# Kernel tuning notes

Hardware: AMD Instinct MI355X
Metric: run time of the kernel (lower is better)

Reference implementation:

```python
import jax, jax.numpy as jnp
import numpy as np
from jax import lax

NH = 8          # heads
DK = 64         # total key/query depth
DV = 64         # total value depth
DKH = DK // NH  # per-head key depth = 8
DVH = DV // NH  # per-head value depth = 8
H = W = 32
CIN = 256
FILTERS = 256


def rel_to_abs(x):
    # x: [B, N, L, 2L-1] relative logits -> [B, N, L, L] absolute logits
    B, N, L, _ = x.shape
    x = jnp.pad(x, ((0, 0), (0, 0), (0, 0), (0, 1)))          # [B,N,L,2L]
    flat = x.reshape(B, N, L * 2 * L)
    flat = jnp.pad(flat, ((0, 0), (0, 0), (0, L - 1)))        # [B,N,2L^2+L-1]
    final = flat.reshape(B, N, L + 1, 2 * L - 1)
    return final[:, :, :L, L - 1:]


def rel_logits_1d(q, rel_k, h, w, perm):
    # q: [B, NH, h, w, DKH], rel_k: [2w-1, DKH]
    B = q.shape[0]
    rel = jnp.einsum('bnxyd,md->bnxym', q, rel_k)             # [B,NH,h,w,2w-1]
    rel = rel.reshape(B, NH * h, w, 2 * w - 1)
    rel = rel_to_abs(rel)                                     # [B,NH*h,w,w]
    rel = rel.reshape(B, NH, h, w, w)[:, :, :, None]          # [B,NH,h,1,w,w]
    rel = jnp.broadcast_to(rel, (B, NH, h, h, w, w))          # tile over other axis
    rel = jnp.transpose(rel, perm)
    return rel.reshape(B, NH, h * w, h * w)


def setup_inputs() -> dict:
    key = jax.random.key(0)
    ks = jax.random.split(key, 6)
    s = lambda fan_in: 1.0 / np.sqrt(fan_in)
    return {
        'x': jax.random.normal(ks[0], (8, H, W, CIN), jnp.float32),
        'conv_w': jax.random.normal(ks[1], (3, 3, CIN, FILTERS - DV), jnp.float32) * s(9 * CIN),
        'conv_b': jnp.zeros((FILTERS - DV,), jnp.float32),
        'qkv_w': jax.random.normal(ks[2], (CIN, 2 * DK + DV), jnp.float32) * s(CIN),
        'qkv_b': jnp.zeros((2 * DK + DV,), jnp.float32),
        'attn_w': jax.random.normal(ks[3], (DV, DV), jnp.float32) * s(DV),
        'attn_b': jnp.zeros((DV,), jnp.float32),
        'key_rel_w': jax.random.normal(ks[4], (2 * W - 1, DKH), jnp.float32),
        'key_rel_h': jax.random.normal(ks[5], (2 * H - 1, DKH), jnp.float32),
    }


def reference(x, conv_w, conv_b, qkv_w, qkv_b, attn_w, attn_b, key_rel_w, key_rel_h):
    B = x.shape[0]
    # standard conv branch (SAME padding)
    conv_out = lax.conv_general_dilated(
        x, conv_w, window_strides=(1, 1), padding='SAME',
        dimension_numbers=('NHWC', 'HWIO', 'NHWC')) + conv_b

    # 1x1 qkv projection
    kqv = jnp.einsum('bhwc,co->bhwo', x, qkv_w) + qkv_b
    k = kqv[..., :DK]
    q = kqv[..., DK:2 * DK] * (DKH ** -0.5)
    v = kqv[..., 2 * DK:]

    def split_heads(t, d):
        return t.reshape(B, H, W, NH, d).transpose(0, 3, 1, 2, 4)  # [B,NH,H,W,d]

    qh = split_heads(q, DKH)
    kh = split_heads(k, DKH)
    vh = split_heads(v, DVH)

    qf = qh.reshape(B, NH, H * W, DKH)
    kf = kh.reshape(B, NH, H * W, DKH)
    vf = vh.reshape(B, NH, H * W, DVH)

    logits = jnp.einsum('bnid,bnjd->bnij', qf, kf)            # [B,NH,HW,HW]
    rel_w = rel_logits_1d(qh, key_rel_w, H, W, (0, 1, 2, 4, 3, 5))
    qh_t = qh.transpose(0, 1, 3, 2, 4)                        # [B,NH,W,H,d]
    rel_h = rel_logits_1d(qh_t, key_rel_h, W, H, (0, 1, 4, 2, 5, 3))
    logits = logits + rel_w + rel_h

    weights = jax.nn.softmax(logits, axis=-1)
    attn = jnp.einsum('bnij,bnjd->bnid', weights, vf)         # [B,NH,HW,DVH]
    attn = attn.reshape(B, NH, H, W, DVH).transpose(0, 2, 3, 1, 4).reshape(B, H, W, DV)
    attn = jnp.einsum('bhwc,co->bhwo', attn, attn_w) + attn_b

    return jnp.concatenate([conv_out, attn], axis=3)
```

## Files before the change

kernel.cpp:

```cpp
#include <hip/hip_runtime.h>
#include <cstdint>

using u16 = unsigned short;
using u32 = uint32_t;

typedef __attribute__((ext_vector_type(8))) short bf16x8;
typedef __attribute__((ext_vector_type(4))) float f32x4;

__device__ __forceinline__ float bf2f(u16 v) { return __uint_as_float(((u32)v) << 16); }
__device__ __forceinline__ u16 f2bf(float f) {
    u32 u = __float_as_uint(f);
    u += 0x7fffu + ((u >> 16) & 1u);
    return (u16)(u >> 16);
}

#define FLAG_OFF 0
#define WSH_OFF  2097168
#define AWF_OFF  2588688
#define CBF_OFF  2592784
#define QBF_OFF  2592976
#define ABF_OFF  2593168
#define KRW_OFF  2593232
#define KRH_OFF  2593736
#define KB_OFF   2594240
#define QB_OFF   3118528
#define VB_OFF   3642816
#define AT_OFF   4167104
#define WSHQ_OFF 9409984

__global__ void detect_kernel(const u16* __restrict__ x, int* __restrict__ flag) {
    __shared__ int cnt;
    if (threadIdx.x == 0) cnt = 0;
    __syncthreads();
    int c = 0;
    #pragma unroll
    for (int k = 0; k < 16; k++) {
        u16 v = x[threadIdx.x * 16 + k];
        int e = (v >> 7) & 0xFF;
        c += (e >= 110 && e <= 140) ? 1 : 0;
    }
    atomicAdd(&cnt, c);
    __syncthreads();
    if (threadIdx.x == 0) *flag = (cnt > 3300) ? 1 : 0;
}

__global__ __launch_bounds__(256) void prep_kernel(
    const void* __restrict__ cw, const void* __restrict__ qw,
    const void* __restrict__ cb, const void* __restrict__ qb,
    const void* __restrict__ aw, const void* __restrict__ ab,
    const void* __restrict__ kw_, const void* __restrict__ kh_,
    u16* __restrict__ wshC, u16* __restrict__ wshQ,
    float* __restrict__ cbf, float* __restrict__ qbf, float* __restrict__ awf,
    float* __restrict__ abf, float* __restrict__ krw, float* __restrict__ krh,
    const int* __restrict__ flag)
{
    const int blk = blockIdx.x;
    const int fl = *flag;
    if (blk < 240) {
        const void* w; u16* o; int g;
        if (blk < 216) { w = cw; o = wshC; g = blk * 256 + threadIdx.x; }
        else           { w = qw; o = wshQ; g = (blk - 216) * 256 + threadIdx.x; }
        const int kk = g / 768, rem = g % 768;
        const int tile = rem >> 6, lane = rem & 63;
        const int n = tile * 16 + (lane & 15);
        u16 tmp[8];
        #pragma unroll
        for (int j = 0; j < 8; j++) {
            const size_t k = (size_t)(kk * 32 + ((lane >> 4) << 3) + j);
            tmp[j] = fl ? ((const u16*)w)[k * 192 + n]
                        : f2bf(((const float*)w)[k * 192 + n]);
        }
        *(uint4*)(o + (size_t)g * 8) = *(const uint4*)tmp;
    } else {
        const int gid = (blk - 240) * 256 + threadIdx.x;
        const void* src; float* dst; int e;
        if      (gid <  192) { src = cb;  dst = cbf; e = gid; }
        else if (gid <  384) { src = qb;  dst = qbf; e = gid - 192; }
        else if (gid < 4480) { src = aw;  dst = awf; e = gid - 384; }
        else if (gid < 4544) { src = ab;  dst = abf; e = gid - 4480; }
        else if (gid < 5048) { src = kw_; dst = krw; e = gid - 4544; }
        else if (gid < 5552) { src = kh_; dst = krh; e = gid - 5048; }
        else return;
        dst[e] = fl ? bf2f(((const u16*)src)[e]) : ((const float*)src)[e];
    }
}

__global__ __launch_bounds__(256) void qkv_mfma_kernel(
    const void* __restrict__ xr, const u16* __restrict__ wsh, const float* __restrict__ qbf_,
    const int* __restrict__ flag,
    u16* __restrict__ kb16, float* __restrict__ qbuf, u16* __restrict__ vb16)
{
    const int coh = blockIdx.x, row = blockIdx.y;
    const int b = row >> 5, h = row & 31;
    const int t = threadIdx.x;
    __shared__ u16 xs[32 * 264];
    const int fl = *flag;

    if (fl) {
        const u16* src = (const u16*)xr + (size_t)row * 8192;
        #pragma unroll
        for (int i = 0; i < 4; ++i) {
            const int idx = t + i * 256;
            const int px = idx >> 5, cq = idx & 31;
            *(uint4*)(xs + px * 264 + cq * 8) = *(const uint4*)(src + px * 256 + cq * 8);
        }
    } else {
        const float* src = (const float*)xr + (size_t)row * 8192;
        #pragma unroll
        for (int i = 0; i < 8; ++i) {
            const int idx = t + i * 256;
            const int px = idx >> 6, c4 = idx & 63;
            float4 v = *(const float4*)(src + px * 256 + c4 * 4);
            u32 lo = (u32)f2bf(v.x) | ((u32)f2bf(v.y) << 16);
            u32 hi = (u32)f2bf(v.z) | ((u32)f2bf(v.w) << 16);
            *(uint2*)(xs + px * 264 + c4 * 4) = make_uint2(lo, hi);
        }
    }
    __syncthreads();

    const int lane = t & 63, wave = t >> 6;
    const int Mtile = wave & 1;
    const int tg0 = coh * 6 + (wave >> 1) * 3;
    const int l15 = lane & 15, quad = lane >> 4;

    f32x4 acc[3] = {{0,0,0,0},{0,0,0,0},{0,0,0,0}};

    const u16* ap = xs + (Mtile * 16 + l15) * 264 + quad * 8;
    #pragma unroll
    for (int kk = 0; kk < 8; ++kk) {
        const bf16x8 av = *(const bf16x8*)(ap + kk * 32);
        const u16* wp = wsh + ((size_t)(kk * 12 + tg0) * 64 + lane) * 8;
        const bf16x8 b0 = *(const bf16x8*)(wp);
        const bf16x8 b1 = *(const bf16x8*)(wp + 512);
        const bf16x8 b2 = *(const bf16x8*)(wp + 1024);
        acc[0] = __builtin_amdgcn_mfma_f32_16x16x32_bf16(av, b0, acc[0], 0, 0, 0);
        acc[1] = __builtin_amdgcn_mfma_f32_16x16x32_bf16(av, b1, acc[1], 0, 0, 0);
        acc[2] = __builtin_amdgcn_mfma_f32_16x16x32_bf16(av, b2, acc[2], 0, 0, 0);
    }

    const int px0 = Mtile * 16 + quad * 4;
    #pragma unroll
    for (int ti = 0; ti < 3; ++ti) {
        const int tg = tg0 + ti;
        const int o = tg * 16 + l15;
        const int third = tg >> 2;
        const int within = o - third * 64;
        const int n = within >> 3, d = within & 7;
        const float bias = qbf_[o];
        #pragma unroll
        for (int r = 0; r < 4; ++r) {
            const int i = h * 32 + px0 + r;
            const size_t off = ((size_t)(b * 8 + n) * 1024 + i) * 8 + d;
            const float val = acc[ti][r] + bias;
            if (third == 0)      kb16[off] = f2bf(val);
            else if (third == 1) qbuf[off] = val * 0.51006973050f;
            else                 vb16[off] = f2bf(val);
        }
    }
}

__global__ __launch_bounds__(256) void conv_mfma_kernel(
    const void* __restrict__ xr, const u16* __restrict__ wsh, const float* __restrict__ cbf,
    const int* __restrict__ flag, void* __restrict__ out)
{
    const int coh = blockIdx.x, row = blockIdx.y;
    const int b = row >> 5, h = row & 31;
    const int t = threadIdx.x;
    __shared__ u16 xs[3 * 34 * 264];
    const int fl = *flag;

    #pragma unroll
    for (int r = 0; r < 3; ++r) {
        const int hh = h + r - 1;
        if (t < 64) {
            const int s = (t >> 5) ? 33 : 0, cq = t & 31;
            *(uint4*)(xs + (r * 34 + s) * 264 + cq * 8) = make_uint4(0, 0, 0, 0);
        }
        const bool ok = (hh >= 0) && (hh < 32);
        const size_t base = ((size_t)((b * 32 + (ok ? hh : 0)) * 32)) * 256;
        if (fl) {
            const u16* src = (const u16*)xr + base;
            #pragma unroll
            for (int i = 0; i < 4; ++i) {
                const int idx = t + i * 256;
                const int px = idx >> 5, cq = idx & 31;
                uint4 v = ok ? *(const uint4*)(src + px * 256 + cq * 8)
                             : make_uint4(0, 0, 0, 0);
                *(uint4*)(xs + (r * 34 + 1 + px) * 264 + cq * 8) = v;
            }
        } else {
            const float* src = (const float*)xr + base;
            #pragma unroll
            for (int i = 0; i < 8; ++i) {
                const int idx = t + i * 256;
                const int px = idx >> 6, c4 = idx & 63;
                float4 v = ok ? *(const float4*)(src + px * 256 + c4 * 4)
                              : make_float4(0.f, 0.f, 0.f, 0.f);
                u32 lo = (u32)f2bf(v.x) | ((u32)f2bf(v.y) << 16);
                u32 hi = (u32)f2bf(v.z) | ((u32)f2bf(v.w) << 16);
                *(uint2*)(xs + (r * 34 + 1 + px) * 264 + c4 * 4) = make_uint2(lo, hi);
            }
        }
    }
    __syncthreads();

    const int lane = t & 63, wave = t >> 6;
    const int Mtile = wave & 1;
    const int tg0 = coh * 6 + (wave >> 1) * 3;
    const int l15 = lane & 15, quad = lane >> 4;

    f32x4 acc[3] = {{0,0,0,0},{0,0,0,0},{0,0,0,0}};

    #pragma unroll
    for (int p = 0; p < 9; ++p) {
        const int kh = p / 3, kw = p - kh * 3;
        const u16* ap = xs + (kh * 34 + kw + Mtile * 16 + l15) * 264 + quad * 8;
        #pragma unroll
        for (int ck = 0; ck < 8; ++ck) {
            const int kk = p * 8 + ck;
            const bf16x8 av = *(const bf16x8*)(ap + ck * 32);
            const u16* wp = wsh + ((size_t)(kk * 12 + tg0) * 64 + lane) * 8;
            const bf16x8 b0 = *(const bf16x8*)(wp);
            const bf16x8 b1 = *(const bf16x8*)(wp + 512);
            const bf16x8 b2 = *(const bf16x8*)(wp + 1024);
            acc[0] = __builtin_amdgcn_mfma_f32_16x16x32_bf16(av, b0, acc[0], 0, 0, 0);
            acc[1] = __builtin_amdgcn_mfma_f32_16x16x32_bf16(av, b1, acc[1], 0, 0, 0);
            acc[2] = __builtin_amdgcn_mfma_f32_16x16x32_bf16(av, b2, acc[2], 0, 0, 0);
        }
    }

    const int px0 = Mtile * 16 + quad * 4;
    #pragma unroll
    for (int ti = 0; ti < 3; ++ti) {
        const int co = (tg0 + ti) * 16 + l15;
        const float bias = cbf[co];
        #pragma unroll
        for (int r = 0; r < 4; ++r) {
            const size_t oidx = ((size_t)row * 32 + px0 + r) * 256 + co;
            const float v = acc[ti][r] + bias;
            if (fl) ((u16*)out)[oidx] = f2bf(v);
            else    ((float*)out)[oidx] = v;
        }
    }
}

__global__ __launch_bounds__(256) void attn_mfma_kernel(
    const u16* __restrict__ kb16, const float* __restrict__ qbuf, const u16* __restrict__ vb16,
    const float* __restrict__ krw, const float* __restrict__ krh, float* __restrict__ attnbuf)
{
    const int qb = blockIdx.x;
    const int bn = blockIdx.y;
    const int b = bn >> 3, hn = bn & 7;
    const int t = threadIdx.x;
    const int i0 = qb * 64;

    __shared__ u16   sVT[8 * 1032];
    __shared__ u16   sRW[64 * 40];
    __shared__ float sRH[32 * 68];
    __shared__ u16   sP [4 * 16 * 56];

    const u16* vg = vb16 + (size_t)bn * 8192;
    #pragma unroll
    for (int k4 = 0; k4 < 4; k4++) {
        const int key = t + k4 * 256;
        uint4 vv = *(const uint4*)(vg + key * 8);
        sVT[0 * 1032 + key] = (u16)(vv.x);  sVT[1 * 1032 + key] = (u16)(vv.x >> 16);
        sVT[2 * 1032 + key] = (u16)(vv.y);  sVT[3 * 1032 + key] = (u16)(vv.y >> 16);
        sVT[4 * 1032 + key] = (u16)(vv.z);  sVT[5 * 1032 + key] = (u16)(vv.z >> 16);
        sVT[6 * 1032 + key] = (u16)(vv.w);  sVT[7 * 1032 + key] = (u16)(vv.w >> 16);
    }
    #pragma unroll
    for (int k8 = 0; k8 < 8; k8++) {
        const int idx = t + k8 * 256;
        const int il = idx >> 5, w = idx & 31;
        const int i = i0 + il;
        const float* q = qbuf + ((size_t)bn * 1024 + i) * 8;
        float4 qa = *(const float4*)q, qc = *(const float4*)(q + 4);
        const float* rp = krw + (size_t)(w - (i & 31) + 31) * 8;
        float4 ra = *(const float4*)rp, rc = *(const float4*)(rp + 4);
        sRW[il * 40 + w] = f2bf(qa.x*ra.x + qa.y*ra.y + qa.z*ra.z + qa.w*ra.w
                              + qc.x*rc.x + qc.y*rc.y + qc.z*rc.z + qc.w*rc.w);
        const float* hp = krh + (size_t)(w - (i >> 5) + 31) * 8;
        float4 ha = *(const float4*)hp, hc = *(const float4*)(hp + 4);
        sRH[w * 68 + il] = qa.x*ha.x + qa.y*ha.y + qa.z*ha.z + qa.w*ha.w
                         + qc.x*hc.x + qc.y*hc.y + qc.z*hc.z + qc.w*hc.w;
    }
    __syncthreads();

    const int lane = t & 63, wave = t >> 6;
    const int l15 = lane & 15, quad = lane >> 4;

    union Frag { u16 a[8]; bf16x8 v; };
    Frag Aq;
    {
        const float* q = qbuf + ((size_t)bn * 1024 + i0 + wave * 16 + l15) * 8;
        float4 qa = *(const float4*)q, qc = *(const float4*)(q + 4);
        Aq.a[0] = f2bf(qa.x); Aq.a[1] = f2bf(qa.y); Aq.a[2] = f2bf(qa.z); Aq.a[3] = f2bf(qa.w);
        Aq.a[4] = f2bf(qc.x); Aq.a[5] = f2bf(qc.y); Aq.a[6] = f2bf(qc.z); Aq.a[7] = f2bf(qc.w);
        if (quad != 0) {
            #pragma unroll
            for (int j = 0; j < 8; j++) Aq.a[j] = 0;
        }
    }
    const bf16x8 Arw = *(const bf16x8*)(sRW + (wave * 16 + l15) * 40 + quad * 8);

    Frag P0, P1, ONE;
    #pragma unroll
    for (int j = 0; j < 8; j++) { P0.a[j] = 0; P1.a[j] = 0; ONE.a[j] = 0x3F80; }
    {
        const int h0 = l15 - quad * 8;
        if (h0 >= 0 && h0 < 8) P0.a[h0] = 0x3F80;
        const int h1 = 16 + l15 - quad * 8;
        if (h1 >= 0 && h1 < 8) P1.a[h1] = 0x3F80;
    }

    const u16* kg = kb16 + (size_t)bn * 8192;
    u16* pb = sP + wave * (16 * 56);
    f32x4 oacc = {0.f, 0.f, 0.f, 0.f};

    for (int chunk = 0; chunk < 32; chunk++) {
        const float4 rh4 = *(const float4*)(sRH + chunk * 68 + wave * 16 + quad * 4);
        f32x4 acc0 = {rh4.x, rh4.y, rh4.z, rh4.w};
        f32x4 acc1 = acc0;
        const bf16x8 bk0 = *(const bf16x8*)(kg + (chunk * 32 + l15) * 8);
        const bf16x8 bk1 = *(const bf16x8*)(kg + (chunk * 32 + 16 + l15) * 8);
        acc0 = __builtin_amdgcn_mfma_f32_16x16x32_bf16(Aq.v, bk0, acc0, 0, 0, 0);
        acc0 = __builtin_amdgcn_mfma_f32_16x16x32_bf16(Arw, P0.v, acc0, 0, 0, 0);
        acc1 = __builtin_amdgcn_mfma_f32_16x16x32_bf16(Aq.v, bk1, acc1, 0, 0, 0);
        acc1 = __builtin_amdgcn_mfma_f32_16x16x32_bf16(Arw, P1.v, acc1, 0, 0, 0);
        #pragma unroll
        for (int r = 0; r < 4; r++) {
            const float p0 = exp2f(fminf(acc0[r], 80.0f));
            const float p1 = exp2f(fminf(acc1[r], 80.0f));
            pb[(quad * 4 + r) * 56 + l15]      = f2bf(p0);
            pb[(quad * 4 + r) * 56 + 16 + l15] = f2bf(p1);
        }
        const bf16x8 Ap = *(const bf16x8*)(pb + l15 * 56 + quad * 8);
        bf16x8 Bv;
        if (l15 < 8) Bv = *(const bf16x8*)(sVT + l15 * 1032 + chunk * 32 + quad * 8);
        else         Bv = ONE.v;
        oacc = __builtin_amdgcn_mfma_f32_16x16x32_bf16(Ap, Bv, oacc, 0, 0, 0);
    }

    #pragma unroll
    for (int r = 0; r < 4; r++) {
        const float lr = __shfl(oacc[r], (lane & 48) | 8, 64);
        const float val = oacc[r] / fmaxf(lr, 1e-30f);
        if (l15 < 8) {
            const int i = i0 + wave * 16 + quad * 4 + r;
            attnbuf[((size_t)b * 1024 + i) * 64 + hn * 8 + l15] = val;
        }
    }
}

__global__ __launch_bounds__(256) void proj_kernel(
    const float* __restrict__ attnbuf, const float* __restrict__ awf, const float* __restrict__ abf,
    const int* __restrict__ flag, void* __restrict__ out)
{
    const int g = blockIdx.x * 256 + threadIdx.x;
    const int px = g >> 6, o = g & 63;
    const float* ar = attnbuf + (size_t)px * 64;
    float acc = abf[o];
    #pragma unroll 8
    for (int c = 0; c < 64; c++) acc += ar[c] * awf[c * 64 + o];
    if (*flag) ((u16*)out)[(size_t)px * 256 + 192 + o] = f2bf(acc);
    else       ((float*)out)[(size_t)px * 256 + 192 + o] = acc;
}

extern "C" void kernel_launch(void* const* d_in, const int* in_sizes, int n_in,
                              void* d_out, int out_size, void* d_ws, size_t ws_size,
                              hipStream_t stream)
{
    float* ws = (float*)d_ws;
    int*   flag = (int*)(ws + FLAG_OFF);
    u16*   wsh  = (u16*)(ws + WSH_OFF);
    float* awf  = ws + AWF_OFF;
    float* cbf  = ws + CBF_OFF;
    float* qbf  = ws + QBF_OFF;
    float* abf  = ws + ABF_OFF;
    float* krw  = ws + KRW_OFF;
    float* krh  = ws + KRH_OFF;
    u16*   kb16 = (u16*)(ws + KB_OFF);
    float* qbuf = ws + QB_OFF;
    u16*   vb16 = (u16*)(ws + VB_OFF);
    float* atb  = ws + AT_OFF;
    u16*   wshQ = (u16*)(ws + WSHQ_OFF);

    detect_kernel<<<1, 256, 0, stream>>>((const u16*)d_in[0], flag);

    prep_kernel<<<262, 256, 0, stream>>>(
        d_in[1], d_in[3], d_in[2], d_in[4], d_in[5], d_in[6], d_in[7], d_in[8],
        wsh, wshQ, cbf, qbf, awf, abf, krw, krh, flag);

    qkv_mfma_kernel <<<dim3(2, 256), 256, 0, stream>>>(d_in[0], wshQ, qbf, flag, kb16, qbuf, vb16);
    conv_mfma_kernel<<<dim3(2, 256), 256, 0, stream>>>(d_in[0], wsh, cbf, flag, d_out);
    attn_mfma_kernel<<<dim3(16, 64), 256, 0, stream>>>(kb16, qbuf, vb16, krw, krh, atb);
    proj_kernel     <<<2048,         256, 0, stream>>>(atb, awf, abf, flag, d_out);
}
```

Baseline: 175.0 us.

## Software-pipeline attention loop with double-buffered P tiles and K prefetch

Restructures the attention inner loop so the logits and exp for chunk c+1 are computed while the PV MFMA for chunk c runs. It does this by double-buffering the per-wave P tile in LDS and prefetching K fragments two chunks ahead in registers. It also switches to the hardware bf16 conversion intrinsic when available and changes the P row stride. The aim is to hide global-load and LDS latency behind MFMA work, at the cost of more registers and LDS. The hardware conversion may differ from the manual rounding in NaN handling.

```diff
diff --git a/kernel.cpp b/kernel.cpp
--- a/kernel.cpp
+++ b/kernel.cpp
@@ -12,6 +12,14 @@
     u32 u = __float_as_uint(f);
     u += 0x7fffu + ((u >> 16) & 1u);
     return (u16)(u >> 16);
+}
+__device__ __forceinline__ u16 bf16u(float f) {
+#if defined(__BF16_MANT_DIG__)
+    __bf16 h = (__bf16)f;
+    return __builtin_bit_cast(u16, h);
+#else
+    return f2bf(f);
+#endif
 }
 
 #define FLAG_OFF 0
@@ -244,6 +252,38 @@
     }
 }
 
+#define ATTN_STEP(C, KA, KB, KA2, KB2)                                          \
+  do {                                                                          \
+    const int c_ = (C);                                                         \
+       \
+    const bf16x8 apf = *(const bf16x8*)(pwb + (c_ & 1) * 640 + l15 * 40 + quad * 8); \
+    bf16x8 bvf;                                                                 \
+    if (l15 < 8) bvf = *(const bf16x8*)(sVT + l15 * 1032 + c_ * 32 + quad * 8); \
+    else         bvf = ONE.v;                                                   \
+    if (c_ + 1 < 32) {                                                          \
+      if (c_ + 2 < 32) {             \
+        KA2 = *(const bf16x8*)(kg + ((c_ + 2) * 32 + l15) * 8);                 \
+        KB2 = *(const bf16x8*)(kg + ((c_ + 2) * 32 + 16 + l15) * 8);            \
+      }                                                                         \
+      const float4 rh4 = *(const float4*)(sRH + (c_ + 1) * 68 + wave * 16 + quad * 4); \
+      f32x4 acc0 = {rh4.x, rh4.y, rh4.z, rh4.w};                                \
+      f32x4 acc1 = acc0;                                                        \
+      acc0 = __builtin_amdgcn_mfma_f32_16x16x32_bf16(Aq.v, KA, acc0, 0, 0, 0);  \
+      acc0 = __builtin_amdgcn_mfma_f32_16x16x32_bf16(Arw, P0.v, acc0, 0, 0, 0); \
+      acc1 = __builtin_amdgcn_mfma_f32_16x16x32_bf16(Aq.v, KB, acc1, 0, 0, 0);  \
+      acc1 = __builtin_amdgcn_mfma_f32_16x16x32_bf16(Arw, P1.v, acc1, 0, 0, 0); \
+      u16* pbn = pwb + ((c_ + 1) & 1) * 640 + l15;                              \
+      _Pragma("unroll")                                                         \
+      for (int r = 0; r < 4; r++) {                                             \
+        const float p0 = exp2f(fminf(acc0[r], 80.0f));                          \
+        const float p1 = exp2f(fminf(acc1[r], 80.0f));                          \
+        pbn[(quad * 4 + r) * 40]      = bf16u(p0);                              \
+        pbn[(quad * 4 + r) * 40 + 16] = bf16u(p1);                              \
+      }                                                                         \
+    }                                                                           \
+    oacc = __builtin_amdgcn_mfma_f32_16x16x32_bf16(apf, bvf, oacc, 0, 0, 0);    \
+  } while (0)
+
 __global__ __launch_bounds__(256) void attn_mfma_kernel(
     const u16* __restrict__ kb16, const float* __restrict__ qbuf, const u16* __restrict__ vb16,
     const float* __restrict__ krw, const float* __restrict__ krh, float* __restrict__ attnbuf)
@@ -254,10 +294,10 @@
     const int t = threadIdx.x;
     const int i0 = qb * 64;
 
-    __shared__ u16   sVT[8 * 1032];
-    __shared__ u16   sRW[64 * 40];
-    __shared__ float sRH[32 * 68];
-    __shared__ u16   sP [4 * 16 * 56];
+    __shared__ __align__(16) u16   sVT[8 * 1032];
+    __shared__ __align__(16) u16   sRW[64 * 40];
+    __shared__ __align__(16) float sRH[32 * 68];
+    __shared__ __align__(16) u16   sP [4 * 1280];
 
     const u16* vg = vb16 + (size_t)bn * 8192;
     #pragma unroll
@@ -315,31 +355,33 @@
     }
 
     const u16* kg = kb16 + (size_t)bn * 8192;
-    u16* pb = sP + wave * (16 * 56);
+    u16* const pwb = sP + wave * 1280;
     f32x4 oacc = {0.f, 0.f, 0.f, 0.f};
-
-    for (int chunk = 0; chunk < 32; chunk++) {
-        const float4 rh4 = *(const float4*)(sRH + chunk * 68 + wave * 16 + quad * 4);
+    bf16x8 kA, kB, kA2, kB2;
+
+    {
+        const bf16x8 k0 = *(const bf16x8*)(kg + l15 * 8);
+        const bf16x8 k1 = *(const bf16x8*)(kg + (16 + l15) * 8);
+        const float4 rh4 = *(const float4*)(sRH + wave * 16 + quad * 4);
         f32x4 acc0 = {rh4.x, rh4.y, rh4.z, rh4.w};
         f32x4 acc1 = acc0;
-        const bf16x8 bk0 = *(const bf16x8*)(kg + (chunk * 32 + l15) * 8);
-        const bf16x8 bk1 = *(const bf16x8*)(kg + (chunk * 32 + 16 + l15) * 8);
-        acc0 = __builtin_amdgcn_mfma_f32_16x16x32_bf16(Aq.v, bk0, acc0, 0, 0, 0);
+        acc0 = __builtin_amdgcn_mfma_f32_16x16x32_bf16(Aq.v, k0, acc0, 0, 0, 0);
         acc0 = __builtin_amdgcn_mfma_f32_16x16x32_bf16(Arw, P0.v, acc0, 0, 0, 0);
-        acc1 = __builtin_amdgcn_mfma_f32_16x16x32_bf16(Aq.v, bk1, acc1, 0, 0, 0);
+        acc1 = __builtin_amdgcn_mfma_f32_16x16x32_bf16(Aq.v, k1, acc1, 0, 0, 0);
         acc1 = __builtin_amdgcn_mfma_f32_16x16x32_bf16(Arw, P1.v, acc1, 0, 0, 0);
+        u16* pbn = pwb + l15;
         #pragma unroll
         for (int r = 0; r < 4; r++) {
-            const float p0 = exp2f(fminf(acc0[r], 80.0f));
-            const float p1 = exp2f(fminf(acc1[r], 80.0f));
-            pb[(quad * 4 + r) * 56 + l15]      = f2bf(p0);
-            pb[(quad * 4 + r) * 56 + 16 + l15] = f2bf(p1);
-        }
-        const bf16x8 Ap = *(const bf16x8*)(pb + l15 * 56 + quad * 8);
-        bf16x8 Bv;
-        if (l15 < 8) Bv = *(const bf16x8*)(sVT + l15 * 1032 + chunk * 32 + quad * 8);
-        else         Bv = ONE.v;
-        oacc = __builtin_amdgcn_mfma_f32_16x16x32_bf16(Ap, Bv, oacc, 0, 0, 0);
+            pbn[(quad * 4 + r) * 40]      = bf16u(exp2f(fminf(acc0[r], 80.0f)));
+            pbn[(quad * 4 + r) * 40 + 16] = bf16u(exp2f(fminf(acc1[r], 80.0f)));
+        }
+        kA = *(const bf16x8*)(kg + (32 + l15) * 8);
+        kB = *(const bf16x8*)(kg + (48 + l15) * 8);
+    }
+
+    for (int c2 = 0; c2 < 32; c2 += 2) {
+        ATTN_STEP(c2,     kA,  kB,  kA2, kB2);
+        ATTN_STEP(c2 + 1, kA2, kB2, kA,  kB);
     }
 
     #pragma unroll
```

New measurement: 173.5 us. No clear change (-0.8%).

## Transpose attention MFMA operands so softmax probabilities stay in registers

Applied to the files above, without the earlier changes.

The attention inner loop now computes the transposed score tile (keys as the A operand, queries as B) with permuted key rows and a reworked selector matrix. The resulting accumulator layout can feed the P·V MFMA directly as the B operand, so the per-chunk LDS round trip for probabilities and its buffer are removed. It also prefetches the next key fragments one iteration ahead, using a zeroed workspace buffer so non-quad-0 lanes read zeros without branching, and uses a native bf16 conversion plus a vectorized float4 output store. The price is more intricate lane and row mapping, which raises correctness risk.

```diff
diff --git a/kernel.cpp b/kernel.cpp
--- a/kernel.cpp
+++ b/kernel.cpp
@@ -13,8 +13,17 @@
     u += 0x7fffu + ((u >> 16) & 1u);
     return (u16)(u >> 16);
 }
+__device__ __forceinline__ u16 bf16u(float f) {
+#if defined(__BF16_MANT_DIG__)
+    __bf16 h = (__bf16)f;
+    return __builtin_bit_cast(u16, h);
+#else
+    return f2bf(f);
+#endif
+}
 
 #define FLAG_OFF 0
+#define ZERO_OFF 8
 #define WSH_OFF  2097168
 #define AWF_OFF  2588688
 #define CBF_OFF  2592784
@@ -52,7 +61,7 @@
     u16* __restrict__ wshC, u16* __restrict__ wshQ,
     float* __restrict__ cbf, float* __restrict__ qbf, float* __restrict__ awf,
     float* __restrict__ abf, float* __restrict__ krw, float* __restrict__ krh,
-    const int* __restrict__ flag)
+    float* __restrict__ zbuf, const int* __restrict__ flag)
 {
     const int blk = blockIdx.x;
     const int fl = *flag;
@@ -80,6 +89,7 @@
         else if (gid < 4544) { src = ab;  dst = abf; e = gid - 4480; }
         else if (gid < 5048) { src = kw_; dst = krw; e = gid - 4544; }
         else if (gid < 5552) { src = kh_; dst = krh; e = gid - 5048; }
+        else if (gid < 5568) { zbuf[gid - 5552] = 0.f; return; }
         else return;
         dst[e] = fl ? bf2f(((const u16*)src)[e]) : ((const float*)src)[e];
     }
@@ -246,7 +256,8 @@
 
 __global__ __launch_bounds__(256) void attn_mfma_kernel(
     const u16* __restrict__ kb16, const float* __restrict__ qbuf, const u16* __restrict__ vb16,
-    const float* __restrict__ krw, const float* __restrict__ krh, float* __restrict__ attnbuf)
+    const float* __restrict__ krw, const float* __restrict__ krh,
+    const u16* __restrict__ zb, float* __restrict__ attnbuf)
 {
     const int qb = blockIdx.x;
     const int bn = blockIdx.y;
@@ -254,10 +265,9 @@
     const int t = threadIdx.x;
     const int i0 = qb * 64;
 
-    __shared__ u16   sVT[8 * 1032];
-    __shared__ u16   sRW[64 * 40];
-    __shared__ float sRH[32 * 68];
-    __shared__ u16   sP [4 * 16 * 56];
+    __shared__ __align__(16) u16   sVT[8 * 1032];
+    __shared__ __align__(16) u16   sRW[64 * 40];
+    __shared__ __align__(16) float sRH[32 * 68];
 
     const u16* vg = vb16 + (size_t)bn * 8192;
     #pragma unroll
@@ -304,52 +314,68 @@
     }
     const bf16x8 Arw = *(const bf16x8*)(sRW + (wave * 16 + l15) * 40 + quad * 8);
 
-    Frag P0, P1, ONE;
-    #pragma unroll
-    for (int j = 0; j < 8; j++) { P0.a[j] = 0; P1.a[j] = 0; ONE.a[j] = 0x3F80; }
-    {
-        const int h0 = l15 - quad * 8;
-        if (h0 >= 0 && h0 < 8) P0.a[h0] = 0x3F80;
-        const int h1 = 16 + l15 - quad * 8;
-        if (h1 >= 0 && h1 < 8) P1.a[h1] = 0x3F80;
+    Frag S0, S1, ONE;
+    #pragma unroll
+    for (int j = 0; j < 8; j++) { S0.a[j] = 0; S1.a[j] = 0; ONE.a[j] = 0x3F80; }
+    if (quad == (l15 >> 2)) {
+        S0.a[l15 & 3]       = 0x3F80;
+        S1.a[4 + (l15 & 3)] = 0x3F80;
     }
 
     const u16* kg = kb16 + (size_t)bn * 8192;
-    u16* pb = sP + wave * (16 * 56);
+    const u16* kp0; const u16* kp1; int kst;
+    if (quad == 0) {
+        const int s = l15 >> 2, r = l15 & 3;
+        kp0 = kg + (size_t)(8 * s + r) * 8;
+        kp1 = kg + (size_t)(8 * s + 4 + r) * 8;
+        kst = 256;
+    } else { kp0 = zb; kp1 = zb; kst = 0; }
+
     f32x4 oacc = {0.f, 0.f, 0.f, 0.f};
 
-    for (int chunk = 0; chunk < 32; chunk++) {
-        const float4 rh4 = *(const float4*)(sRH + chunk * 68 + wave * 16 + quad * 4);
-        f32x4 acc0 = {rh4.x, rh4.y, rh4.z, rh4.w};
+    bf16x8 kA = *(const bf16x8*)kp0;
+    bf16x8 kB = *(const bf16x8*)kp1;
+
+    for (int c = 0; c < 32; ++c) {
+        bf16x8 kA2 = kA, kB2 = kB;
+        if (c + 1 < 32) {
+            kA2 = *(const bf16x8*)(kp0 + kst);
+            kB2 = *(const bf16x8*)(kp1 + kst);
+            kp0 += kst; kp1 += kst;
+        }
+        const float rhv = sRH[c * 68 + wave * 16 + l15];
+        f32x4 acc0 = {rhv, rhv, rhv, rhv};
         f32x4 acc1 = acc0;
-        const bf16x8 bk0 = *(const bf16x8*)(kg + (chunk * 32 + l15) * 8);
-        const bf16x8 bk1 = *(const bf16x8*)(kg + (chunk * 32 + 16 + l15) * 8);
-        acc0 = __builtin_amdgcn_mfma_f32_16x16x32_bf16(Aq.v, bk0, acc0, 0, 0, 0);
-        acc0 = __builtin_amdgcn_mfma_f32_16x16x32_bf16(Arw, P0.v, acc0, 0, 0, 0);
-        acc1 = __builtin_amdgcn_mfma_f32_16x16x32_bf16(Aq.v, bk1, acc1, 0, 0, 0);
-        acc1 = __builtin_amdgcn_mfma_f32_16x16x32_bf16(Arw, P1.v, acc1, 0, 0, 0);
-        #pragma unroll
-        for (int r = 0; r < 4; r++) {
-            const float p0 = exp2f(fminf(acc0[r], 80.0f));
-            const float p1 = exp2f(fminf(acc1[r], 80.0f));
-            pb[(quad * 4 + r) * 56 + l15]      = f2bf(p0);
-            pb[(quad * 4 + r) * 56 + 16 + l15] = f2bf(p1);
-        }
-        const bf16x8 Ap = *(const bf16x8*)(pb + l15 * 56 + quad * 8);
-        bf16x8 Bv;
-        if (l15 < 8) Bv = *(const bf16x8*)(sVT + l15 * 1032 + chunk * 32 + quad * 8);
-        else         Bv = ONE.v;
-        oacc = __builtin_amdgcn_mfma_f32_16x16x32_bf16(Ap, Bv, oacc, 0, 0, 0);
-    }
-
-    #pragma unroll
-    for (int r = 0; r < 4; r++) {
-        const float lr = __shfl(oacc[r], (lane & 48) | 8, 64);
-        const float val = oacc[r] / fmaxf(lr, 1e-30f);
-        if (l15 < 8) {
-            const int i = i0 + wave * 16 + quad * 4 + r;
-            attnbuf[((size_t)b * 1024 + i) * 64 + hn * 8 + l15] = val;
-        }
+        acc0 = __builtin_amdgcn_mfma_f32_16x16x32_bf16(kA,   Aq.v, acc0, 0, 0, 0);
+        acc0 = __builtin_amdgcn_mfma_f32_16x16x32_bf16(S0.v, Arw,  acc0, 0, 0, 0);
+        acc1 = __builtin_amdgcn_mfma_f32_16x16x32_bf16(kB,   Aq.v, acc1, 0, 0, 0);
+        acc1 = __builtin_amdgcn_mfma_f32_16x16x32_bf16(S1.v, Arw,  acc1, 0, 0, 0);
+        kA = kA2; kB = kB2;
+
+        union { u16 a[8]; bf16x8 v; } pf;
+        pf.a[0] = bf16u(exp2f(fminf(acc0[0], 80.0f)));
+        pf.a[1] = bf16u(exp2f(fminf(acc0[1], 80.0f)));
+        pf.a[2] = bf16u(exp2f(fminf(acc0[2], 80.0f)));
+        pf.a[3] = bf16u(exp2f(fminf(acc0[3], 80.0f)));
+        pf.a[4] = bf16u(exp2f(fminf(acc1[0], 80.0f)));
+        pf.a[5] = bf16u(exp2f(fminf(acc1[1], 80.0f)));
+        pf.a[6] = bf16u(exp2f(fminf(acc1[2], 80.0f)));
+        pf.a[7] = bf16u(exp2f(fminf(acc1[3], 80.0f)));
+
+        bf16x8 Av;
+        if (l15 < 8) Av = *(const bf16x8*)(sVT + l15 * 1032 + c * 32 + quad * 8);
+        else         Av = ONE.v;
+        oacc = __builtin_amdgcn_mfma_f32_16x16x32_bf16(Av, pf.v, oacc, 0, 0, 0);
+    }
+
+    const float lr = __shfl(oacc[0], 32 + l15, 64);
+    const float inv = 1.0f / fmaxf(lr, 1e-30f);
+    if (quad < 2) {
+        float4 o;
+        o.x = oacc[0] * inv; o.y = oacc[1] * inv;
+        o.z = oacc[2] * inv; o.w = oacc[3] * inv;
+        *(float4*)(attnbuf + ((size_t)b * 1024 + i0 + wave * 16 + l15) * 64
+                   + hn * 8 + quad * 4) = o;
     }
 }
 
@@ -373,6 +399,7 @@
 {
     float* ws = (float*)d_ws;
     int*   flag = (int*)(ws + FLAG_OFF);
+    float* zbuf = ws + ZERO_OFF;
     u16*   wsh  = (u16*)(ws + WSH_OFF);
     float* awf  = ws + AWF_OFF;
     float* cbf  = ws + CBF_OFF;
@@ -390,10 +417,11 @@
 
     prep_kernel<<<262, 256, 0, stream>>>(
         d_in[1], d_in[3], d_in[2], d_in[4], d_in[5], d_in[6], d_in[7], d_in[8],
-        wsh, wshQ, cbf, qbf, awf, abf, krw, krh, flag);
+        wsh, wshQ, cbf, qbf, awf, abf, krw, krh, zbuf, flag);
 
     qkv_mfma_kernel <<<dim3(2, 256), 256, 0, stream>>>(d_in[0], wshQ, qbf, flag, kb16, qbuf, vb16);
     conv_mfma_kernel<<<dim3(2, 256), 256, 0, stream>>>(d_in[0], wsh, cbf, flag, d_out);
-    attn_mfma_kernel<<<dim3(16, 64), 256, 0, stream>>>(kb16, qbuf, vb16, krw, krh, atb);
+    attn_mfma_kernel<<<dim3(16, 64), 256, 0, stream>>>(kb16, qbuf, vb16, krw, krh,
+                                                       (const u16*)zbuf, atb);
     proj_kernel     <<<2048,         256, 0, stream>>>(atb, awf, abf, flag, d_out);
 }
```

New measurement: 178.0 us. No clear change (+1.7%).
